# Optimization experiments

Measured on AMD Instinct MI355X. Metric: run time of the kernel, lower is better.

Reference implementation:

```python
import jax, jax.numpy as jnp
import numpy as np

VOCAB, EMB, HID, OUT = 128, 128, 256, 2
B, T = 128, 2048


def setup_inputs() -> dict:
    key = jax.random.key(0)
    ks = jax.random.split(key, 8)
    s_ih = 1.0 / np.sqrt(HID)
    inp = {
        "x": jax.random.randint(ks[0], (B, T), 0, VOCAB, dtype=jnp.int32),
        "emb": jax.random.normal(ks[1], (VOCAB, EMB), jnp.float32),
        "W_ih": jax.random.uniform(ks[2], (4 * HID, EMB), jnp.float32, -s_ih, s_ih),
        "W_hh": jax.random.uniform(ks[3], (4 * HID, HID), jnp.float32, -s_ih, s_ih),
        "b_ih": jax.random.uniform(ks[4], (4 * HID,), jnp.float32, -s_ih, s_ih),
        "b_hh": jax.random.uniform(ks[5], (4 * HID,), jnp.float32, -s_ih, s_ih),
        "fc_W": jax.random.normal(ks[6], (OUT, HID), jnp.float32) * np.sqrt(6.0 / (HID + OUT)),
        "fc_b": jnp.zeros((OUT,), jnp.float32),
    }
    return inp


def _lstm_last_hidden(xe, W_ih, W_hh, b_ih, b_hh):
    # xe: [B, T, E]. Precompute all input-to-hidden gate projections (batched GEMM).
    Bsz = xe.shape[0]
    H = W_hh.shape[1]
    xg = jnp.einsum('bte,ge->tbg', xe, W_ih) + (b_ih + b_hh)  # [T, B, 4H]

    def step(carry, xt):
        h, c = carry
        g = xt + h @ W_hh.T                 # [B, 4H]
        i, f, gg, o = jnp.split(g, 4, axis=-1)  # PyTorch gate order i,f,g,o
        i = jax.nn.sigmoid(i)
        f = jax.nn.sigmoid(f)
        gg = jnp.tanh(gg)
        o = jax.nn.sigmoid(o)
        c = f * c + i * gg
        h = o * jnp.tanh(c)
        return (h, c), None

    h0 = jnp.zeros((Bsz, H), xe.dtype)
    c0 = jnp.zeros((Bsz, H), xe.dtype)
    (hT, _), _ = jax.lax.scan(step, (h0, c0), xg)
    return hT  # == output[:, -1, :] for a uni-directional LSTM


def reference(x, emb, W_ih, W_hh, b_ih, b_hh, fc_W, fc_b):
    xe = emb[x]                                   # [B, T, E] embedding lookup
    hT = _lstm_last_hidden(xe, W_ih, W_hh, b_ih, b_hh)
    logits = hT @ fc_W.T + fc_b                   # [B, OUT]
    return logits
```

## Files before the change

kernel.cpp:

```cpp
#include <hip/hip_runtime.h>

#define T_LEN 2048
#define HID   256
#define G4    1024
#define EMBD  128
#define VOCAB 128
#define OUTC  2
#define BSUB  2
#define NWG   64
#define HSB   288
#define LOG2E 1.44269504088896340736f

typedef int   i32x4 __attribute__((ext_vector_type(4)));
typedef float f32x4 __attribute__((ext_vector_type(4)));

__device__ __align__(16) float Pbuf[VOCAB * G4];
__device__ __align__(16) signed char Wqb[G4 * HID];
__device__ float Winv[G4];

__global__ void build_P(const float* __restrict__ emb, const float* __restrict__ W_ih,
                        const float* __restrict__ b_ih, const float* __restrict__ b_hh) {
    const int v = blockIdx.x >> 2;
    const int c = ((blockIdx.x & 3) << 8) + threadIdx.x;
    __shared__ float es[EMBD];
    if (threadIdx.x < EMBD) es[threadIdx.x] = emb[v * EMBD + threadIdx.x];
    __syncthreads();
    const float* wr = W_ih + c * EMBD;
    float acc = 0.f;
    #pragma unroll 8
    for (int e = 0; e < EMBD; ++e) acc += es[e] * wr[e];
    const float ks = ((c >> 8) == 2) ? (-2.f * LOG2E) : (-LOG2E);
    const int g  = c >> 8;
    const int rr = c & 255;
    const int wi = rr >> 5;
    const int nt = (rr >> 4) & 1;
    const int l  = rr & 15;
    Pbuf[v * G4 + wi * 128 + nt * 64 + l * 4 + g] = (acc + b_ih[c] + b_hh[c]) * ks;
}

__global__ void quant_W(const float* __restrict__ W_hh) {
    const int row = blockIdx.x;
    const int k   = threadIdx.x;
    __shared__ float red[4];
    const float wv = W_hh[row * HID + k];
    float a = fabsf(wv);
    #pragma unroll
    for (int o = 32; o > 0; o >>= 1) a = fmaxf(a, __shfl_down(a, o, 64));
    if ((k & 63) == 0) red[k >> 6] = a;
    __syncthreads();
    const float m = fmaxf(fmaxf(fmaxf(red[0], red[1]), red[2]), fmaxf(red[3], 1e-30f));
    Wqb[row * HID + k] = (signed char)(int)rintf(wv * (127.f / m));
    const float ks = ((row >> 8) == 2) ? (-2.f * LOG2E) : (-LOG2E);
    if (k == 0) Winv[row] = m * (1.f / (127.f * 127.f)) * ks;
}

__global__ __launch_bounds__(512, 2) void lstm_chain(
        const int* __restrict__ x, const float* __restrict__ fc_W,
        const float* __restrict__ fc_b, float* __restrict__ out) {
    __shared__ __align__(16) signed char habuf[2][BSUB * HSB];
    __shared__ __align__(16) int xls[BSUB][T_LEN];
    __shared__ float hfin[BSUB * HID];

    const int tid  = threadIdx.x;
    const int w    = tid >> 6;
    const int lane = tid & 63;
    const int l15  = lane & 15;
    const int quad = lane >> 4;
    const int bbase = blockIdx.x * BSUB;
    const int ub    = w * 32;
    const int bq    = quad >> 1;
    const int ntq   = quad & 1;
    const int colq  = ub + ntq * 16 + l15;

    i32x4 Bf[2][4][4];
    #pragma unroll
    for (int nt = 0; nt < 2; ++nt)
        #pragma unroll
        for (int g = 0; g < 4; ++g) {
            const signed char* wr = Wqb + (size_t)(g * HID + ub + nt * 16 + l15) * HID;
            #pragma unroll
            for (int kt = 0; kt < 4; ++kt)
                Bf[nt][g][kt] = *(const i32x4*)(wr + kt * 64 + quad * 16);
        }
    float winvv[4];
    #pragma unroll
    for (int g = 0; g < 4; ++g) winvv[g] = Winv[g * HID + colq];

    {
        const i32x4* xsrc = (const i32x4*)(x + (size_t)bbase * T_LEN);
        i32x4* xdst = (i32x4*)xls;
        i32x4 v0 = xsrc[tid];
        i32x4 v1 = xsrc[tid + 512];
        #pragma unroll
        for (int j = 0; j < 4; ++j) { v0[j] <<= 12; v1[j] <<= 12; }
        xdst[tid]       = v0;
        xdst[tid + 512] = v1;
    }
    if (tid < BSUB * HSB / 4) ((int*)habuf[0])[tid] = 0;

    float cst = 0.f;
    f32x4 xga, xgb;
    const i32x4 zero4 = {0, 0, 0, 0};
    const char* pbase = (const char*)(Pbuf + w * 128 + ntq * 64 + l15 * 4);
    const signed char* habA = habuf[0] + (l15 >> 3) * HSB + quad * 16;
    const signed char* habB = habuf[1] + (l15 >> 3) * HSB + quad * 16;

#define GATHER(TT, XG)                                                        \
    {                                                                         \
        const int xo = xls[bq][(TT)];                                         \
        XG = *(const f32x4*)(pbase + xo);                                     \
    }

#define STEP(HAB, HN, XC, XN, PF, TT, TCUR)                                   \
    {                                                                         \
        i32x4 af[4];                                                          \
        _Pragma("unroll")                                                     \
        for (int kt = 0; kt < 4; ++kt)                                        \
            af[kt] = *(const i32x4*)((HAB) + kt * 64);                        \
        if (PF) GATHER((TT), XN);                                             \
        i32x4 a0[4], a1[4];                                                   \
        _Pragma("unroll")                                                     \
        for (int g = 0; g < 4; ++g)                                           \
            a0[g] = __builtin_amdgcn_mfma_i32_16x16x64_i8(af[0], Bf[0][g][0], zero4, 0, 0, 0); \
        _Pragma("unroll")                                                     \
        for (int kt = 1; kt < 4; ++kt)                                        \
            _Pragma("unroll")                                                 \
            for (int g = 0; g < 4; ++g)                                       \
                a0[g] = __builtin_amdgcn_mfma_i32_16x16x64_i8(af[kt], Bf[0][g][kt], a0[g], 0, 0, 0); \
        _Pragma("unroll")                                                     \
        for (int g = 0; g < 4; ++g)                                           \
            a1[g] = __builtin_amdgcn_mfma_i32_16x16x64_i8(af[0], Bf[1][g][0], zero4, 0, 0, 0); \
        _Pragma("unroll")                                                     \
        for (int kt = 1; kt < 4; ++kt)                                        \
            _Pragma("unroll")                                                 \
            for (int g = 0; g < 4; ++g)                                       \
                a1[g] = __builtin_amdgcn_mfma_i32_16x16x64_i8(af[kt], Bf[1][g][kt], a1[g], 0, 0, 0); \
             \
        const int gi_ = ntq ? a1[0][0] : a0[0][0];                            \
        const int gf_ = ntq ? a1[1][0] : a0[1][0];                            \
        const int gg_ = ntq ? a1[2][0] : a0[2][0];                            \
        const int go_ = ntq ? a1[3][0] : a0[3][0];                            \
        const float pi = fmaf((float)gi_, winvv[0], XC[0]);                   \
        const float pf = fmaf((float)gf_, winvv[1], XC[1]);                   \
        const float pg = fmaf((float)gg_, winvv[2], XC[2]);                   \
        const float po = fmaf((float)go_, winvv[3], XC[3]);                   \
        const float Ei = __builtin_amdgcn_exp2f(pi);                          \
        const float Ef = __builtin_amdgcn_exp2f(pf);                          \
        const float Eg = __builtin_amdgcn_exp2f(pg);                          \
        const float Eo = __builtin_amdgcn_exp2f(po);                          \
        const float Aig = (1.f + Ei) * (1.f + Eg);                            \
        const float R3  = __builtin_amdgcn_rcpf(Aig * (1.f + Ef));            \
        const float fs  = Aig * R3;                             \
        const float ig  = (1.f + Ef) * R3 * (1.f - Eg);   \
        const float c   = fmaf(fs, cst, ig);                                  \
        cst = c;                                                              \
        const float Ec  = __builtin_amdgcn_exp2f(fminf(c * (-2.f * LOG2E), 60.f)); \
        const float R2  = __builtin_amdgcn_rcpf((1.f + Eo) * (1.f + Ec));     \
        const float hq  = fmaf(-127.f, Ec, 127.f) * R2;    \
        (HN)[bq * HSB + colq] = (signed char)(int)rintf(hq);                  \
        if ((TCUR) == T_LEN - 1) hfin[bq * HID + colq] = hq * (1.f / 127.f);  \
        __syncthreads();                                                      \
    }

    __syncthreads();
    GATHER(0, xga);
    #pragma unroll 1
    for (int tt = 0; tt < T_LEN; tt += 2) {
        STEP(habA, habuf[1], xga, xgb, 1, tt + 1, tt);
        STEP(habB, habuf[0], xgb, xga, (tt < T_LEN - 2), tt + 2, tt + 1);
    }
#undef STEP
#undef GATHER

    if (tid < BSUB * OUTC) {
        const int b = tid >> 1, o = tid & 1;
        float s = fc_b[o];
        #pragma unroll 8
        for (int j = 0; j < HID; ++j) s += hfin[b * HID + j] * fc_W[o * HID + j];
        out[(bbase + b) * OUTC + o] = s;
    }
}

extern "C" void kernel_launch(void* const* d_in, const int* in_sizes, int n_in,
                              void* d_out, int out_size, void* d_ws, size_t ws_size,
                              hipStream_t stream) {
    const int*   x    = (const int*)  d_in[0];
    const float* emb  = (const float*)d_in[1];
    const float* W_ih = (const float*)d_in[2];
    const float* W_hh = (const float*)d_in[3];
    const float* b_ih = (const float*)d_in[4];
    const float* b_hh = (const float*)d_in[5];
    const float* fc_W = (const float*)d_in[6];
    const float* fc_b = (const float*)d_in[7];
    float* out = (float*)d_out;
    (void)d_ws; (void)ws_size;

    build_P<<<dim3(VOCAB * 4), dim3(256), 0, stream>>>(emb, W_ih, b_ih, b_hh);
    quant_W<<<dim3(G4), dim3(HID), 0, stream>>>(W_hh);
    lstm_chain<<<dim3(NWG), dim3(512), 0, stream>>>(x, fc_W, fc_b, out);
}
```

Before: 1.418 ms.

## Split LSTM recurrence across 16 waves with one column tile per wave

```diff
diff --git a/kernel.cpp b/kernel.cpp
--- a/kernel.cpp
+++ b/kernel.cpp
@@ -30,12 +30,9 @@
     #pragma unroll 8
     for (int e = 0; e < EMBD; ++e) acc += es[e] * wr[e];
     const float ks = ((c >> 8) == 2) ? (-2.f * LOG2E) : (-LOG2E);
-    const int g  = c >> 8;
-    const int rr = c & 255;
-    const int wi = rr >> 5;
-    const int nt = (rr >> 4) & 1;
-    const int l  = rr & 15;
-    Pbuf[v * G4 + wi * 128 + nt * 64 + l * 4 + g] = (acc + b_ih[c] + b_hh[c]) * ks;
+    const int g = c >> 8;
+    const int u = c & 255;
+    Pbuf[v * G4 + u * 4 + g] = (acc + b_ih[c] + b_hh[c]) * ks;
 }
 
 __global__ void quant_W(const float* __restrict__ W_hh) {
@@ -54,7 +51,7 @@
     if (k == 0) Winv[row] = m * (1.f / (127.f * 127.f)) * ks;
 }
 
-__global__ __launch_bounds__(512, 2) void lstm_chain(
+__global__ __launch_bounds__(1024, 4) void lstm_chain(
         const int* __restrict__ x, const float* __restrict__ fc_W,
         const float* __restrict__ fc_b, float* __restrict__ out) {
     __shared__ __align__(16) signed char habuf[2][BSUB * HSB];
@@ -67,41 +64,35 @@
     const int l15  = lane & 15;
     const int quad = lane >> 4;
     const int bbase = blockIdx.x * BSUB;
-    const int ub    = w * 32;
+    const int colq  = w * 16 + l15;
     const int bq    = quad >> 1;
-    const int ntq   = quad & 1;
-    const int colq  = ub + ntq * 16 + l15;
+    const bool wact = !(quad & 1);
 
-    i32x4 Bf[2][4][4];
+    i32x4 Bf[4][4];
     #pragma unroll
-    for (int nt = 0; nt < 2; ++nt)
+    for (int g = 0; g < 4; ++g) {
+        const signed char* wr = Wqb + (size_t)(g * HID + colq) * HID;
         #pragma unroll
-        for (int g = 0; g < 4; ++g) {
-            const signed char* wr = Wqb + (size_t)(g * HID + ub + nt * 16 + l15) * HID;
-            #pragma unroll
-            for (int kt = 0; kt < 4; ++kt)
-                Bf[nt][g][kt] = *(const i32x4*)(wr + kt * 64 + quad * 16);
-        }
+        for (int kt = 0; kt < 4; ++kt)
+            Bf[g][kt] = *(const i32x4*)(wr + kt * 64 + quad * 16);
+    }
     float winvv[4];
     #pragma unroll
     for (int g = 0; g < 4; ++g) winvv[g] = Winv[g * HID + colq];
 
     {
         const i32x4* xsrc = (const i32x4*)(x + (size_t)bbase * T_LEN);
-        i32x4* xdst = (i32x4*)xls;
         i32x4 v0 = xsrc[tid];
-        i32x4 v1 = xsrc[tid + 512];
         #pragma unroll
-        for (int j = 0; j < 4; ++j) { v0[j] <<= 12; v1[j] <<= 12; }
-        xdst[tid]       = v0;
-        xdst[tid + 512] = v1;
+        for (int j = 0; j < 4; ++j) v0[j] <<= 12;
+        ((i32x4*)xls)[tid] = v0;
     }
     if (tid < BSUB * HSB / 4) ((int*)habuf[0])[tid] = 0;
 
     float cst = 0.f;
     f32x4 xga, xgb;
     const i32x4 zero4 = {0, 0, 0, 0};
-    const char* pbase = (const char*)(Pbuf + w * 128 + ntq * 64 + l15 * 4);
+    const char* pbase = (const char*)(Pbuf + colq * 4);
     const signed char* habA = habuf[0] + (l15 >> 3) * HSB + quad * 16;
     const signed char* habB = habuf[1] + (l15 >> 3) * HSB + quad * 16;
 
@@ -113,37 +104,24 @@
 
 #define STEP(HAB, HN, XC, XN, PF, TT, TCUR)                                   \
     {                                                                         \
-        i32x4 af[4];                                                          \
-        _Pragma("unroll")                                                     \
-        for (int kt = 0; kt < 4; ++kt)                                        \
-            af[kt] = *(const i32x4*)((HAB) + kt * 64);                        \
+        const i32x4 af0 = *(const i32x4*)(HAB);                               \
         if (PF) GATHER((TT), XN);                                             \
-        i32x4 a0[4], a1[4];                                                   \
+        i32x4 a[4];                                                           \
         _Pragma("unroll")                                                     \
         for (int g = 0; g < 4; ++g)                                           \
-            a0[g] = __builtin_amdgcn_mfma_i32_16x16x64_i8(af[0], Bf[0][g][0], zero4, 0, 0, 0); \
+            a[g] = __builtin_amdgcn_mfma_i32_16x16x64_i8(af0, Bf[g][0], zero4, 0, 0, 0); \
         _Pragma("unroll")                                                     \
-        for (int kt = 1; kt < 4; ++kt)                                        \
+        for (int kt = 1; kt < 4; ++kt) {                                      \
+            const i32x4 afk = *(const i32x4*)((HAB) + kt * 64);               \
             _Pragma("unroll")                                                 \
             for (int g = 0; g < 4; ++g)                                       \
-                a0[g] = __builtin_amdgcn_mfma_i32_16x16x64_i8(af[kt], Bf[0][g][kt], a0[g], 0, 0, 0); \
-        _Pragma("unroll")                                                     \
-        for (int g = 0; g < 4; ++g)                                           \
-            a1[g] = __builtin_amdgcn_mfma_i32_16x16x64_i8(af[0], Bf[1][g][0], zero4, 0, 0, 0); \
-        _Pragma("unroll")                                                     \
-        for (int kt = 1; kt < 4; ++kt)                                        \
-            _Pragma("unroll")                                                 \
-            for (int g = 0; g < 4; ++g)                                       \
-                a1[g] = __builtin_amdgcn_mfma_i32_16x16x64_i8(af[kt], Bf[1][g][kt], a1[g], 0, 0, 0); \
-             \
-        const int gi_ = ntq ? a1[0][0] : a0[0][0];                            \
-        const int gf_ = ntq ? a1[1][0] : a0[1][0];                            \
-        const int gg_ = ntq ? a1[2][0] : a0[2][0];                            \
-        const int go_ = ntq ? a1[3][0] : a0[3][0];                            \
-        const float pi = fmaf((float)gi_, winvv[0], XC[0]);                   \
-        const float pf = fmaf((float)gf_, winvv[1], XC[1]);                   \
-        const float pg = fmaf((float)gg_, winvv[2], XC[2]);                   \
-        const float po = fmaf((float)go_, winvv[3], XC[3]);                   \
+                a[g] = __builtin_amdgcn_mfma_i32_16x16x64_i8(afk, Bf[g][kt], a[g], 0, 0, 0); \
+        }                                                                     \
+                   \
+        const float pi = fmaf((float)a[0][0], winvv[0], XC[0]);               \
+        const float pf = fmaf((float)a[1][0], winvv[1], XC[1]);               \
+        const float pg = fmaf((float)a[2][0], winvv[2], XC[2]);               \
+        const float po = fmaf((float)a[3][0], winvv[3], XC[3]);               \
         const float Ei = __builtin_amdgcn_exp2f(pi);                          \
         const float Ef = __builtin_amdgcn_exp2f(pf);                          \
         const float Eg = __builtin_amdgcn_exp2f(pg);                          \
@@ -157,8 +135,10 @@
         const float Ec  = __builtin_amdgcn_exp2f(fminf(c * (-2.f * LOG2E), 60.f)); \
         const float R2  = __builtin_amdgcn_rcpf((1.f + Eo) * (1.f + Ec));     \
         const float hq  = fmaf(-127.f, Ec, 127.f) * R2;    \
-        (HN)[bq * HSB + colq] = (signed char)(int)rintf(hq);                  \
-        if ((TCUR) == T_LEN - 1) hfin[bq * HID + colq] = hq * (1.f / 127.f);  \
+        if (wact) {                                                           \
+            (HN)[bq * HSB + colq] = (signed char)(int)rintf(hq);              \
+            if ((TCUR) == T_LEN - 1) hfin[bq * HID + colq] = hq * (1.f / 127.f); \
+        }                                                                     \
         __syncthreads();                                                      \
     }
 
@@ -197,5 +177,5 @@
 
     build_P<<<dim3(VOCAB * 4), dim3(256), 0, stream>>>(emb, W_ih, b_ih, b_hh);
     quant_W<<<dim3(G4), dim3(HID), 0, stream>>>(W_hh);
-    lstm_chain<<<dim3(NWG), dim3(512), 0, stream>>>(x, fc_W, fc_b, out);
+    lstm_chain<<<dim3(NWG), dim3(1024), 0, stream>>>(x, fc_W, fc_b, out);
 }
```

Measured after the change: 1.490 ms. 1.05x slower.

## Replace per-step workgroup barrier with per-wave LDS flag handshakes and staggered k-order

Applied to the files above, without the earlier changes.

```diff
diff --git a/kernel.cpp b/kernel.cpp
--- a/kernel.cpp
+++ b/kernel.cpp
@@ -60,6 +60,7 @@
     __shared__ __align__(16) signed char habuf[2][BSUB * HSB];
     __shared__ __align__(16) int xls[BSUB][T_LEN];
     __shared__ float hfin[BSUB * HID];
+    __shared__ int flg[2][8];
 
     const int tid  = threadIdx.x;
     const int w    = tid >> 6;
@@ -71,6 +72,7 @@
     const int bq    = quad >> 1;
     const int ntq   = quad & 1;
     const int colq  = ub + ntq * 16 + l15;
+    const int cw    = w >> 1;
 
     i32x4 Bf[2][4][4];
     #pragma unroll
@@ -97,6 +99,7 @@
         xdst[tid + 512] = v1;
     }
     if (tid < BSUB * HSB / 4) ((int*)habuf[0])[tid] = 0;
+    if (tid < 16) ((volatile int*)flg)[tid] = (tid < 8) ? 0 : -1;
 
     float cst = 0.f;
     f32x4 xga, xgb;
@@ -105,36 +108,55 @@
     const signed char* habA = habuf[0] + (l15 >> 3) * HSB + quad * 16;
     const signed char* habB = habuf[1] + (l15 >> 3) * HSB + quad * 16;
 
+#define WAITF(FB, KT, E)                                                      \
+    {                                                                         \
+        const volatile int* fp_ = &flg[FB][0];                                \
+        while (fp_[2 * (KT)] < (E) || fp_[2 * (KT) + 1] < (E))                \
+            __builtin_amdgcn_s_sleep(1);                                      \
+        __builtin_amdgcn_fence(__ATOMIC_ACQUIRE, "workgroup");                \
+        __builtin_amdgcn_sched_barrier(0);                                    \
+    }
+
+#define PUBLISH(FB, E)                                                        \
+    {                                                                         \
+        __builtin_amdgcn_fence(__ATOMIC_RELEASE, "workgroup");                \
+        if (lane == 0) ((volatile int*)flg[FB])[w] = (E);                     \
+        __builtin_amdgcn_sched_barrier(0);                                    \
+    }
+
 #define GATHER(TT, XG)                                                        \
     {                                                                         \
         const int xo = xls[bq][(TT)];                                         \
         XG = *(const f32x4*)(pbase + xo);                                     \
     }
 
-#define STEP(HAB, HN, XC, XN, PF, TT, TCUR)                                   \
-    {                                                                         \
-        i32x4 af[4];                                                          \
-        _Pragma("unroll")                                                     \
-        for (int kt = 0; kt < 4; ++kt)                                        \
-            af[kt] = *(const i32x4*)((HAB) + kt * 64);                        \
+#define KBATCH(HAB, FR, EIN, KT, FIRST)                                       \
+    {                                                                         \
+        WAITF(FR, KT, EIN);                                                   \
+        const i32x4 afk = *(const i32x4*)((HAB) + (KT) * 64);                 \
+        if (FIRST) {                                                          \
+            _Pragma("unroll")                                                 \
+            for (int g = 0; g < 4; ++g) {                                     \
+                a0[g] = __builtin_amdgcn_mfma_i32_16x16x64_i8(afk, Bf[0][g][KT], zero4, 0, 0, 0); \
+                a1[g] = __builtin_amdgcn_mfma_i32_16x16x64_i8(afk, Bf[1][g][KT], zero4, 0, 0, 0); \
+            }                                                                 \
+        } else {                                                              \
+            _Pragma("unroll")                                                 \
+            for (int g = 0; g < 4; ++g) {                                     \
+                a0[g] = __builtin_amdgcn_mfma_i32_16x16x64_i8(afk, Bf[0][g][KT], a0[g], 0, 0, 0); \
+                a1[g] = __builtin_amdgcn_mfma_i32_16x16x64_i8(afk, Bf[1][g][KT], a1[g], 0, 0, 0); \
+            }                                                                 \
+        }                                                                     \
+    }
+
+#define STEP(HAB, HN, XC, XN, PF, TT, TCUR, FR, FW, EIN, EOUT, K0, K1, K2, K3)\
+    {                                                                         \
+        i32x4 a0[4], a1[4];                                                   \
+        KBATCH(HAB, FR, EIN, K0, 1);                                          \
         if (PF) GATHER((TT), XN);                                             \
-        i32x4 a0[4], a1[4];                                                   \
-        _Pragma("unroll")                                                     \
-        for (int g = 0; g < 4; ++g)                                           \
-            a0[g] = __builtin_amdgcn_mfma_i32_16x16x64_i8(af[0], Bf[0][g][0], zero4, 0, 0, 0); \
-        _Pragma("unroll")                                                     \
-        for (int kt = 1; kt < 4; ++kt)                                        \
-            _Pragma("unroll")                                                 \
-            for (int g = 0; g < 4; ++g)                                       \
-                a0[g] = __builtin_amdgcn_mfma_i32_16x16x64_i8(af[kt], Bf[0][g][kt], a0[g], 0, 0, 0); \
-        _Pragma("unroll")                                                     \
-        for (int g = 0; g < 4; ++g)                                           \
-            a1[g] = __builtin_amdgcn_mfma_i32_16x16x64_i8(af[0], Bf[1][g][0], zero4, 0, 0, 0); \
-        _Pragma("unroll")                                                     \
-        for (int kt = 1; kt < 4; ++kt)                                        \
-            _Pragma("unroll")                                                 \
-            for (int g = 0; g < 4; ++g)                                       \
-                a1[g] = __builtin_amdgcn_mfma_i32_16x16x64_i8(af[kt], Bf[1][g][kt], a1[g], 0, 0, 0); \
+        KBATCH(HAB, FR, EIN, K1, 0);                                          \
+        KBATCH(HAB, FR, EIN, K2, 0);                                          \
+        KBATCH(HAB, FR, EIN, K3, 0);                                          \
              \
         const int gi_ = ntq ? a1[0][0] : a0[0][0];                            \
         const int gf_ = ntq ? a1[1][0] : a0[1][0];                            \
@@ -159,18 +181,34 @@
         const float hq  = fmaf(-127.f, Ec, 127.f) * R2;    \
         (HN)[bq * HSB + colq] = (signed char)(int)rintf(hq);                  \
         if ((TCUR) == T_LEN - 1) hfin[bq * HID + colq] = hq * (1.f / 127.f);  \
-        __syncthreads();                                                      \
-    }
-
-    __syncthreads();
-    GATHER(0, xga);
-    #pragma unroll 1
-    for (int tt = 0; tt < T_LEN; tt += 2) {
-        STEP(habA, habuf[1], xga, xgb, 1, tt + 1, tt);
-        STEP(habB, habuf[0], xgb, xga, (tt < T_LEN - 2), tt + 2, tt + 1);
-    }
+        PUBLISH(FW, EOUT);                                                    \
+    }
+
+#define RUNLOOP(K0, K1, K2, K3)                                               \
+    {                                                                         \
+        GATHER(0, xga);                                                       \
+        _Pragma("unroll 1")                                                   \
+        for (int tt = 0; tt < T_LEN; tt += 2) {                               \
+            const int inst = tt >> 1;                                         \
+            STEP(habA, habuf[1], xga, xgb, 1, tt + 1, tt,                     \
+                 0, 1, inst, inst, K0, K1, K2, K3);                           \
+            STEP(habB, habuf[0], xgb, xga, (tt < T_LEN - 2), tt + 2, tt + 1,  \
+                 1, 0, inst, inst + 1, K0, K1, K2, K3);                       \
+        }                                                                     \
+    }
+
+    __syncthreads();
+    if      (cw == 0) RUNLOOP(0, 1, 2, 3)
+    else if (cw == 1) RUNLOOP(1, 2, 3, 0)
+    else if (cw == 2) RUNLOOP(2, 3, 0, 1)
+    else              RUNLOOP(3, 0, 1, 2)
+    __syncthreads();
+#undef RUNLOOP
 #undef STEP
+#undef KBATCH
 #undef GATHER
+#undef PUBLISH
+#undef WAITF
 
     if (tid < BSUB * OUTC) {
         const int b = tid >> 1, o = tid & 1;
```

Result: slower. 2.312 ms (+63.1%).
